# Optimization experiments

Hardware: AMD Instinct MI355X
Metric: run time of the kernel (lower is better)

Reference implementation:

```python
import jax, jax.numpy as jnp
import numpy as np

N_NODES = 50000
N_EDGES = 800000
D = 128  # hidden_channels == num_filters
SHIFT = float(np.log(2.0))


def shifted_softplus(x):
    return jax.nn.softplus(x) - SHIFT


def setup_inputs() -> dict:
    key = jax.random.key(0)
    k1, k2, k3, k4, k5 = jax.random.split(key, 5)
    v = jax.random.normal(k1, (N_NODES, D), dtype=jnp.float32)
    e = jax.random.normal(k2, (N_EDGES, D), dtype=jnp.float32)
    edge_index = jax.random.randint(k3, (2, N_EDGES), 0, N_NODES, dtype=jnp.int64)
    # Xavier-uniform weights, zero biases (as in reset_parameters)
    limit = float(np.sqrt(6.0 / (D + D)))
    W1 = jax.random.uniform(k4, (D, D), minval=-limit, maxval=limit, dtype=jnp.float32)
    b1 = jnp.zeros((D,), dtype=jnp.float32)
    W2 = jax.random.uniform(k5, (D, D), minval=-limit, maxval=limit, dtype=jnp.float32)
    b2 = jnp.zeros((D,), dtype=jnp.float32)
    return {"v": v, "e": e, "edge_index": edge_index,
            "W1": W1, "b1": b1, "W2": W2, "b2": b2}


def reference(v, e, edge_index, W1, b1, W2, b2):
    i = edge_index[1]  # destination node per edge, [E]
    # scatter-sum edge messages into nodes: [N, D]
    agg = jax.ops.segment_sum(e, i, num_segments=v.shape[0])
    h = shifted_softplus(agg @ W1.T + b1)  # lin1 + act (dropout = identity)
    out = h @ W2.T + b2                    # lin2
    return v + out
```

## Files before the change

kernel.cpp:

```cpp
#include <hip/hip_runtime.h>
#include <cstdint>
#include <cstddef>

#define D 128
#define CAP 64

typedef float f4v __attribute__((ext_vector_type(4)));

static __device__ __forceinline__ float ssp(float x) {
    float ax = fabsf(x);
    return fmaxf(x, 0.0f) + log1pf(__expf(-ax)) - 0.6931471805599453f;
}

__global__ void build_lists(const int* __restrict__ ei, int E,
                            int* __restrict__ cnt, int* __restrict__ slots) {
    int t = blockIdx.x * blockDim.x + threadIdx.x;
    if (t < E) {
        int dst = ei[E + t];
        int slot = atomicAdd(&cnt[dst], 1);
        if (slot < CAP) slots[(size_t)dst * CAP + slot] = t;
    }
}

__global__ void transpose_w(const float* __restrict__ W1, const float* __restrict__ W2,
                            float* __restrict__ WT1, float* __restrict__ WT2) {
    const float* W  = blockIdx.y ? W2 : W1;
    float*       WT = blockIdx.y ? WT2 : WT1;
    int j = blockIdx.x;
    int k = threadIdx.x;
    WT[k * D + j] = W[j * D + k];
}

static __device__ __forceinline__ void fma4x4(const float4 a, const float4 w0,
                                              const float4 w1, const float4 w2,
                                              const float4 w3, float4& c) {
    c.x = fmaf(a.x, w0.x, fmaf(a.y, w1.x, fmaf(a.z, w2.x, fmaf(a.w, w3.x, c.x))));
    c.y = fmaf(a.x, w0.y, fmaf(a.y, w1.y, fmaf(a.z, w2.y, fmaf(a.w, w3.y, c.y))));
    c.z = fmaf(a.x, w0.z, fmaf(a.y, w1.z, fmaf(a.z, w2.z, fmaf(a.w, w3.z, c.z))));
    c.w = fmaf(a.x, w0.w, fmaf(a.y, w1.w, fmaf(a.z, w2.w, fmaf(a.w, w3.w, c.w))));
}

static __device__ __forceinline__ int pickEid(const int2 eid2, int idx) {
    int v = (idx & 1) ? eid2.y : eid2.x;
    return __shfl(v, idx >> 1, 32);
}

static __device__ __forceinline__ f4v ldnt(const float* p) {
    return __builtin_nontemporal_load((const f4v*)p);
}

__global__ __launch_bounds__(256) void fused_gather_mlp(
    const float* __restrict__ e, const int* __restrict__ cnt,
    const int* __restrict__ slots, const float* __restrict__ vin,
    const float* __restrict__ WT1, const float* __restrict__ b1,
    const float* __restrict__ WT2, const float* __restrict__ b2,
    float* __restrict__ out, int N) {
    __shared__ float As[32][D];
    __shared__ float Hs[32][D];
    const int tid  = threadIdx.x;
    const int row0 = blockIdx.x * 32;
    const int half = tid >> 5;
    const int l32  = tid & 31;

    for (int r = half; r < 32; r += 8) {
        const int n = row0 + r;
        f4v s0 = 0.f, s1 = 0.f, s2 = 0.f, s3 = 0.f;
        if (n < N) {
            int c = cnt[n];
            if (c > CAP) c = CAP;
            const int2 eid2 = ((const int2*)(slots + (size_t)n * CAP))[l32];
            int j = 0;
            for (; j + 8 <= c; j += 8) {
                int e0 = pickEid(eid2, j + 0);
                int e1 = pickEid(eid2, j + 1);
                int e2 = pickEid(eid2, j + 2);
                int e3 = pickEid(eid2, j + 3);
                int e4 = pickEid(eid2, j + 4);
                int e5 = pickEid(eid2, j + 5);
                int e6 = pickEid(eid2, j + 6);
                int e7 = pickEid(eid2, j + 7);
                f4v x0 = ldnt(e + (size_t)e0 * D + l32 * 4);
                f4v x1 = ldnt(e + (size_t)e1 * D + l32 * 4);
                f4v x2 = ldnt(e + (size_t)e2 * D + l32 * 4);
                f4v x3 = ldnt(e + (size_t)e3 * D + l32 * 4);
                f4v x4 = ldnt(e + (size_t)e4 * D + l32 * 4);
                f4v x5 = ldnt(e + (size_t)e5 * D + l32 * 4);
                f4v x6 = ldnt(e + (size_t)e6 * D + l32 * 4);
                f4v x7 = ldnt(e + (size_t)e7 * D + l32 * 4);
                s0 += x0; s1 += x1; s2 += x2; s3 += x3;
                s0 += x4; s1 += x5; s2 += x6; s3 += x7;
            }
            for (; j < c; j += 4) {
                const int  i1 = (j + 1 < c) ? j + 1 : j;
                const int  i2 = (j + 2 < c) ? j + 2 : j;
                const int  i3 = (j + 3 < c) ? j + 3 : j;
                const float w1 = (j + 1 < c) ? 1.f : 0.f;
                const float w2 = (j + 2 < c) ? 1.f : 0.f;
                const float w3 = (j + 3 < c) ? 1.f : 0.f;
                int e0 = pickEid(eid2, j);
                int e1 = pickEid(eid2, i1);
                int e2 = pickEid(eid2, i2);
                int e3 = pickEid(eid2, i3);
                f4v x0 = ldnt(e + (size_t)e0 * D + l32 * 4);
                f4v x1 = ldnt(e + (size_t)e1 * D + l32 * 4);
                f4v x2 = ldnt(e + (size_t)e2 * D + l32 * 4);
                f4v x3 = ldnt(e + (size_t)e3 * D + l32 * 4);
                s0 += x0;
                s1 += x1 * w1;
                s2 += x2 * w2;
                s3 += x3 * w3;
            }
        }
        f4v t4 = (s0 + s1) + (s2 + s3);
        *((f4v*)(&As[r][0]) + l32) = t4;
    }
    __syncthreads();

    const int jg = (tid & 31) << 2;
    const int rg = (tid >> 5) << 2;

    float4 acc[4];
    #pragma unroll
    for (int r = 0; r < 4; ++r) acc[r] = make_float4(0.f, 0.f, 0.f, 0.f);

    for (int k = 0; k < D; k += 4) {
        float4 w0 = *(const float4*)(WT1 + (k + 0) * D + jg);
        float4 w1 = *(const float4*)(WT1 + (k + 1) * D + jg);
        float4 w2 = *(const float4*)(WT1 + (k + 2) * D + jg);
        float4 w3 = *(const float4*)(WT1 + (k + 3) * D + jg);
        #pragma unroll
        for (int r = 0; r < 4; ++r) {
            float4 a = *(const float4*)(&As[rg + r][k]);
            fma4x4(a, w0, w1, w2, w3, acc[r]);
        }
    }
    {
        float4 bb = *(const float4*)(b1 + jg);
        #pragma unroll
        for (int r = 0; r < 4; ++r) {
            float4 h;
            h.x = ssp(acc[r].x + bb.x);
            h.y = ssp(acc[r].y + bb.y);
            h.z = ssp(acc[r].z + bb.z);
            h.w = ssp(acc[r].w + bb.w);
            *(float4*)(&Hs[rg + r][jg]) = h;
        }
    }
    __syncthreads();

    #pragma unroll
    for (int r = 0; r < 4; ++r) acc[r] = make_float4(0.f, 0.f, 0.f, 0.f);

    for (int k = 0; k < D; k += 4) {
        float4 w0 = *(const float4*)(WT2 + (k + 0) * D + jg);
        float4 w1 = *(const float4*)(WT2 + (k + 1) * D + jg);
        float4 w2 = *(const float4*)(WT2 + (k + 2) * D + jg);
        float4 w3 = *(const float4*)(WT2 + (k + 3) * D + jg);
        #pragma unroll
        for (int r = 0; r < 4; ++r) {
            float4 a = *(const float4*)(&Hs[rg + r][k]);
            fma4x4(a, w0, w1, w2, w3, acc[r]);
        }
    }
    {
        float4 bb = *(const float4*)(b2 + jg);
        #pragma unroll
        for (int r = 0; r < 4; ++r) {
            int row = row0 + rg + r;
            if (row < N) {
                float4 vv = *(const float4*)(vin + (size_t)row * D + jg);
                float4 o;
                o.x = vv.x + acc[r].x + bb.x;
                o.y = vv.y + acc[r].y + bb.y;
                o.z = vv.z + acc[r].z + bb.z;
                o.w = vv.w + acc[r].w + bb.w;
                *(float4*)(out + (size_t)row * D + jg) = o;
            }
        }
    }
}

extern "C" void kernel_launch(void* const* d_in, const int* in_sizes, int n_in,
                              void* d_out, int out_size, void* d_ws, size_t ws_size,
                              hipStream_t stream) {
    const float* v  = (const float*)d_in[0];
    const float* e  = (const float*)d_in[1];
    const int*   ei = (const int*)d_in[2];
    const float* W1 = (const float*)d_in[3];
    const float* b1 = (const float*)d_in[4];
    const float* W2 = (const float*)d_in[5];
    const float* b2 = (const float*)d_in[6];

    const int N = in_sizes[0] / D;
    const int E = in_sizes[1] / D;

    char*  ws  = (char*)d_ws;
    size_t off = 0;
    auto alloc = [&](size_t bytes) {
        void* p = ws + off;
        off += (bytes + 255) & ~(size_t)255;
        return p;
    };
    int*   cnt   = (int*)alloc((size_t)N * 4);
    int*   slots = (int*)alloc((size_t)N * CAP * 4);
    float* WT1   = (float*)alloc((size_t)D * D * 4);
    float* WT2   = (float*)alloc((size_t)D * D * 4);
    (void)ws_size; (void)n_in; (void)out_size;

    hipMemsetAsync(cnt, 0, (size_t)N * sizeof(int), stream);
    build_lists<<<(E + 255) / 256, 256, 0, stream>>>(ei, E, cnt, slots);
    transpose_w<<<dim3(D, 2), D, 0, stream>>>(W1, W2, WT1, WT2);
    fused_gather_mlp<<<(N + 31) / 32, 256, 0, stream>>>(
        e, cnt, slots, v, WT1, b1, WT2, b2, (float*)d_out, N);
}
```

Before: 662.8 us.

## Balance gather rows dynamically, drop H buffer, merge setup kernels

The weight transpose and the count zeroing are merged into one setup kernel, replacing a memset and a separate transpose launch. In the gather phase, each 32-lane group now takes rows from a shared-memory ticket counter instead of a fixed stride, which balances the uneven per-node edge counts within a block. The hidden activations reuse the A tile in shared memory, halving LDS use and removing one barrier to raise occupancy. Nontemporal loads and stores are used for edge indices, v and out. Dropping the barrier relies on each row group being handled entirely within one wave64, so it depends on lockstep execution within a wavefront.

```diff
diff --git a/kernel.cpp b/kernel.cpp
--- a/kernel.cpp
+++ b/kernel.cpp
@@ -10,34 +10,32 @@
 static __device__ __forceinline__ float ssp(float x) {
     float ax = fabsf(x);
     return fmaxf(x, 0.0f) + log1pf(__expf(-ax)) - 0.6931471805599453f;
+}
+
+__global__ void setup(const float* __restrict__ W1, const float* __restrict__ W2,
+                      float* __restrict__ WT1, float* __restrict__ WT2,
+                      int* __restrict__ cnt, int N) {
+    int b = blockIdx.x;
+    if (b < 2) {
+        const float* W  = b ? W2 : W1;
+        float*       WT = b ? WT2 : WT1;
+        for (int idx = threadIdx.x; idx < D * D; idx += 256) {
+            WT[idx] = W[((idx & (D - 1)) << 7) | (idx >> 7)];
+        }
+    } else {
+        int i = (b - 2) * 256 + threadIdx.x;
+        if (i < N) cnt[i] = 0;
+    }
 }
 
 __global__ void build_lists(const int* __restrict__ ei, int E,
                             int* __restrict__ cnt, int* __restrict__ slots) {
     int t = blockIdx.x * blockDim.x + threadIdx.x;
     if (t < E) {
-        int dst = ei[E + t];
+        int dst = __builtin_nontemporal_load(ei + E + t);
         int slot = atomicAdd(&cnt[dst], 1);
         if (slot < CAP) slots[(size_t)dst * CAP + slot] = t;
     }
-}
-
-__global__ void transpose_w(const float* __restrict__ W1, const float* __restrict__ W2,
-                            float* __restrict__ WT1, float* __restrict__ WT2) {
-    const float* W  = blockIdx.y ? W2 : W1;
-    float*       WT = blockIdx.y ? WT2 : WT1;
-    int j = blockIdx.x;
-    int k = threadIdx.x;
-    WT[k * D + j] = W[j * D + k];
-}
-
-static __device__ __forceinline__ void fma4x4(const float4 a, const float4 w0,
-                                              const float4 w1, const float4 w2,
-                                              const float4 w3, float4& c) {
-    c.x = fmaf(a.x, w0.x, fmaf(a.y, w1.x, fmaf(a.z, w2.x, fmaf(a.w, w3.x, c.x))));
-    c.y = fmaf(a.x, w0.y, fmaf(a.y, w1.y, fmaf(a.z, w2.y, fmaf(a.w, w3.y, c.y))));
-    c.z = fmaf(a.x, w0.z, fmaf(a.y, w1.z, fmaf(a.z, w2.z, fmaf(a.w, w3.z, c.z))));
-    c.w = fmaf(a.x, w0.w, fmaf(a.y, w1.w, fmaf(a.z, w2.w, fmaf(a.w, w3.w, c.w))));
 }
 
 static __device__ __forceinline__ int pickEid(const int2 eid2, int idx) {
@@ -55,14 +53,20 @@
     const float* __restrict__ WT1, const float* __restrict__ b1,
     const float* __restrict__ WT2, const float* __restrict__ b2,
     float* __restrict__ out, int N) {
-    __shared__ float As[32][D];
-    __shared__ float Hs[32][D];
+    __shared__ __align__(16) float As[32][D];
+    __shared__ int ticket;
     const int tid  = threadIdx.x;
     const int row0 = blockIdx.x * 32;
-    const int half = tid >> 5;
     const int l32  = tid & 31;
 
-    for (int r = half; r < 32; r += 8) {
+    if (tid == 0) ticket = 0;
+    __syncthreads();
+
+    for (;;) {
+        int r = 0;
+        if (l32 == 0) r = atomicAdd(&ticket, 1);
+        r = __shfl(r, 0, 32);
+        if (r >= 32) break;
         const int n = row0 + r;
         f4v s0 = 0.f, s1 = 0.f, s2 = 0.f, s3 = 0.f;
         if (n < N) {
@@ -119,63 +123,71 @@
     const int jg = (tid & 31) << 2;
     const int rg = (tid >> 5) << 2;
 
-    float4 acc[4];
-    #pragma unroll
-    for (int r = 0; r < 4; ++r) acc[r] = make_float4(0.f, 0.f, 0.f, 0.f);
-
+    f4v acc0 = 0.f, acc1 = 0.f, acc2 = 0.f, acc3 = 0.f;
     for (int k = 0; k < D; k += 4) {
-        float4 w0 = *(const float4*)(WT1 + (k + 0) * D + jg);
-        float4 w1 = *(const float4*)(WT1 + (k + 1) * D + jg);
-        float4 w2 = *(const float4*)(WT1 + (k + 2) * D + jg);
-        float4 w3 = *(const float4*)(WT1 + (k + 3) * D + jg);
-        #pragma unroll
-        for (int r = 0; r < 4; ++r) {
-            float4 a = *(const float4*)(&As[rg + r][k]);
-            fma4x4(a, w0, w1, w2, w3, acc[r]);
-        }
+        f4v w0 = *(const f4v*)(WT1 + (size_t)(k + 0) * D + jg);
+        f4v w1 = *(const f4v*)(WT1 + (size_t)(k + 1) * D + jg);
+        f4v w2 = *(const f4v*)(WT1 + (size_t)(k + 2) * D + jg);
+        f4v w3 = *(const f4v*)(WT1 + (size_t)(k + 3) * D + jg);
+        f4v a0 = *(const f4v*)(&As[rg + 0][k]);
+        f4v a1 = *(const f4v*)(&As[rg + 1][k]);
+        f4v a2 = *(const f4v*)(&As[rg + 2][k]);
+        f4v a3 = *(const f4v*)(&As[rg + 3][k]);
+        acc0 += a0.x * w0; acc0 += a0.y * w1; acc0 += a0.z * w2; acc0 += a0.w * w3;
+        acc1 += a1.x * w0; acc1 += a1.y * w1; acc1 += a1.z * w2; acc1 += a1.w * w3;
+        acc2 += a2.x * w0; acc2 += a2.y * w1; acc2 += a2.z * w2; acc2 += a2.w * w3;
+        acc3 += a3.x * w0; acc3 += a3.y * w1; acc3 += a3.z * w2; acc3 += a3.w * w3;
     }
     {
-        float4 bb = *(const float4*)(b1 + jg);
-        #pragma unroll
-        for (int r = 0; r < 4; ++r) {
-            float4 h;
-            h.x = ssp(acc[r].x + bb.x);
-            h.y = ssp(acc[r].y + bb.y);
-            h.z = ssp(acc[r].z + bb.z);
-            h.w = ssp(acc[r].w + bb.w);
-            *(float4*)(&Hs[rg + r][jg]) = h;
-        }
-    }
-    __syncthreads();
-
-    #pragma unroll
-    for (int r = 0; r < 4; ++r) acc[r] = make_float4(0.f, 0.f, 0.f, 0.f);
-
+        f4v bb = *(const f4v*)(b1 + jg);
+        f4v h0 = acc0 + bb, h1 = acc1 + bb, h2 = acc2 + bb, h3 = acc3 + bb;
+        h0.x = ssp(h0.x); h0.y = ssp(h0.y); h0.z = ssp(h0.z); h0.w = ssp(h0.w);
+        h1.x = ssp(h1.x); h1.y = ssp(h1.y); h1.z = ssp(h1.z); h1.w = ssp(h1.w);
+        h2.x = ssp(h2.x); h2.y = ssp(h2.y); h2.z = ssp(h2.z); h2.w = ssp(h2.w);
+        h3.x = ssp(h3.x); h3.y = ssp(h3.y); h3.z = ssp(h3.z); h3.w = ssp(h3.w);
+        *(f4v*)(&As[rg + 0][jg]) = h0;
+        *(f4v*)(&As[rg + 1][jg]) = h1;
+        *(f4v*)(&As[rg + 2][jg]) = h2;
+        *(f4v*)(&As[rg + 3][jg]) = h3;
+    }
+
+    acc0 = 0.f; acc1 = 0.f; acc2 = 0.f; acc3 = 0.f;
     for (int k = 0; k < D; k += 4) {
-        float4 w0 = *(const float4*)(WT2 + (k + 0) * D + jg);
-        float4 w1 = *(const float4*)(WT2 + (k + 1) * D + jg);
-        float4 w2 = *(const float4*)(WT2 + (k + 2) * D + jg);
-        float4 w3 = *(const float4*)(WT2 + (k + 3) * D + jg);
-        #pragma unroll
-        for (int r = 0; r < 4; ++r) {
-            float4 a = *(const float4*)(&Hs[rg + r][k]);
-            fma4x4(a, w0, w1, w2, w3, acc[r]);
-        }
+        f4v w0 = *(const f4v*)(WT2 + (size_t)(k + 0) * D + jg);
+        f4v w1 = *(const f4v*)(WT2 + (size_t)(k + 1) * D + jg);
+        f4v w2 = *(const f4v*)(WT2 + (size_t)(k + 2) * D + jg);
+        f4v w3 = *(const f4v*)(WT2 + (size_t)(k + 3) * D + jg);
+        f4v a0 = *(const f4v*)(&As[rg + 0][k]);
+        f4v a1 = *(const f4v*)(&As[rg + 1][k]);
+        f4v a2 = *(const f4v*)(&As[rg + 2][k]);
+        f4v a3 = *(const f4v*)(&As[rg + 3][k]);
+        acc0 += a0.x * w0; acc0 += a0.y * w1; acc0 += a0.z * w2; acc0 += a0.w * w3;
+        acc1 += a1.x * w0; acc1 += a1.y * w1; acc1 += a1.z * w2; acc1 += a1.w * w3;
+        acc2 += a2.x * w0; acc2 += a2.y * w1; acc2 += a2.z * w2; acc2 += a2.w * w3;
+        acc3 += a3.x * w0; acc3 += a3.y * w1; acc3 += a3.z * w2; acc3 += a3.w * w3;
     }
     {
-        float4 bb = *(const float4*)(b2 + jg);
-        #pragma unroll
-        for (int r = 0; r < 4; ++r) {
-            int row = row0 + rg + r;
-            if (row < N) {
-                float4 vv = *(const float4*)(vin + (size_t)row * D + jg);
-                float4 o;
-                o.x = vv.x + acc[r].x + bb.x;
-                o.y = vv.y + acc[r].y + bb.y;
-                o.z = vv.z + acc[r].z + bb.z;
-                o.w = vv.w + acc[r].w + bb.w;
-                *(float4*)(out + (size_t)row * D + jg) = o;
-            }
+        f4v bb = *(const f4v*)(b2 + jg);
+        const int r0 = row0 + rg;
+        if (r0 + 0 < N) {
+            f4v vv = ldnt(vin + (size_t)(r0 + 0) * D + jg);
+            f4v o = vv + acc0 + bb;
+            __builtin_nontemporal_store(o, (f4v*)(out + (size_t)(r0 + 0) * D + jg));
+        }
+        if (r0 + 1 < N) {
+            f4v vv = ldnt(vin + (size_t)(r0 + 1) * D + jg);
+            f4v o = vv + acc1 + bb;
+            __builtin_nontemporal_store(o, (f4v*)(out + (size_t)(r0 + 1) * D + jg));
+        }
+        if (r0 + 2 < N) {
+            f4v vv = ldnt(vin + (size_t)(r0 + 2) * D + jg);
+            f4v o = vv + acc2 + bb;
+            __builtin_nontemporal_store(o, (f4v*)(out + (size_t)(r0 + 2) * D + jg));
+        }
+        if (r0 + 3 < N) {
+            f4v vv = ldnt(vin + (size_t)(r0 + 3) * D + jg);
+            f4v o = vv + acc3 + bb;
+            __builtin_nontemporal_store(o, (f4v*)(out + (size_t)(r0 + 3) * D + jg));
         }
     }
 }
@@ -207,9 +219,8 @@
     float* WT2   = (float*)alloc((size_t)D * D * 4);
     (void)ws_size; (void)n_in; (void)out_size;
 
-    hipMemsetAsync(cnt, 0, (size_t)N * sizeof(int), stream);
+    setup<<<2 + (N + 255) / 256, 256, 0, stream>>>(W1, W2, WT1, WT2, cnt, N);
     build_lists<<<(E + 255) / 256, 256, 0, stream>>>(ei, E, cnt, slots);
-    transpose_w<<<dim3(D, 2), D, 0, stream>>>(W1, W2, WT1, WT2);
     fused_gather_mlp<<<(N + 31) / 32, 256, 0, stream>>>(
         e, cnt, slots, v, WT1, b1, WT2, b2, (float*)d_out, N);
 }
```

Result: no change. 667.1 us (+0.6%).
